# Optimization experiments

Hardware: AMD Instinct MI355X
Metric: run time of the kernel (lower is better)

The kernel has to match this reference:

```python
import jax, jax.numpy as jnp
import numpy as np

B, S, D, H, NK = 2, 512, 256, 8, 16
DK = D // H
NEG = -1e32


def _layer_norm(x, g, b, eps=1e-5):
    m = jnp.mean(x, axis=-1, keepdims=True)
    v = jnp.var(x, axis=-1, keepdims=True)
    return (x - m) / jnp.sqrt(v + eps) * g + b


def _attention(q, k, v, mask, gamma, maxout):
    # q,k,v: [b,h,s,dk]; mask: [1,1,s,s] bool; gamma: [h,1,1]
    d_k = q.shape[-1]
    scores = jnp.einsum('bhqd,bhkd->bhqk', q, k) / float(np.sqrt(d_k))
    s = scores.shape[-1]
    # gamma exp-decay branch (at=None in practice -> position_effect path)
    sm = jax.nn.softmax(jnp.where(mask, scores, NEG), axis=-1)
    distcum = jnp.cumsum(sm, axis=-1)
    disttotal = jnp.sum(sm, axis=-1, keepdims=True)
    idx = jnp.arange(s, dtype=scores.dtype)
    pos = jnp.abs(idx[None, :] - idx[:, None])[None, None]  # |x1 - x2|
    dist = jax.lax.stop_gradient(
        jnp.sqrt(jnp.clip((disttotal - distcum) * pos, 0.0, None)))
    g = -jnp.abs(gamma)[None]  # [1,h,1,1]
    total_effect = jnp.clip(jnp.exp(dist * g), 1e-5, 1e5)
    scores = scores * total_effect
    scores = jax.nn.softmax(jnp.where(mask, scores, NEG), axis=-1)
    scores = jnp.where(mask, scores, 0.0)
    if maxout:
        scale = jnp.minimum(1.0 / jnp.max(scores, axis=-1, keepdims=True), 5.0)
        scores = scores * scale
    out = jnp.einsum('bhqk,bhkd->bhqd', scores, v)
    return out, scores


def _mha(qx, kx, vx, mask, Wq, bq, Wk, bk, Wv, bv, Wo, bo, gammas, maxout):
    b, s, d = qx.shape
    def proj(x, W, bb):
        return (x @ W.T + bb).reshape(b, s, H, DK).transpose(0, 2, 1, 3)
    q = proj(qx, Wq, bq)
    k = proj(kx, Wk, bk)
    v = proj(vx, Wv, bv)
    out, scores = _attention(q, k, v, mask, gammas, maxout)
    concat = out.transpose(0, 2, 1, 3).reshape(b, s, d)
    return concat @ Wo.T + bo, scores


def _layer(qx, kx, vx, mask, Wq, bq, Wk, bk, Wv, bv, Wo, bo, gammas, ln_g, ln_b, maxout):
    out, scores = _mha(qx, kx, vx, mask, Wq, bq, Wk, bk, Wv, bv, Wo, bo, gammas, maxout)
    return _layer_norm(qx + out, ln_g, ln_b), scores  # dropout=identity in eval


def setup_inputs() -> dict:
    key = jax.random.key(0)
    ks = iter(jax.random.split(key, 40))
    def W(shp, sc=0.05):
        return jax.random.normal(next(ks), shp, jnp.float32) * sc
    return dict(
        q_emb=jax.random.normal(next(ks), (B, S, D), jnp.float32),
        s_emb=jax.random.normal(next(ks), (B, S, D), jnp.float32),
        s_emb_extr=jax.random.normal(next(ks), (B, S, D), jnp.float32),
        lens=jax.random.randint(next(ks), (B,), 1, S),
        at=jax.random.randint(next(ks), (B, S), 0, 300),
        Wq1=W((D, D)), bq1=jnp.zeros((D,)), Wv1=W((D, D)), bv1=jnp.zeros((D,)),
        Wo1=W((D, D)), bo1=jnp.zeros((D,)), gam1=W((H, 1, 1), 0.3),
        ln1_g=jnp.ones((D,)), ln1_b=jnp.zeros((D,)),
        Wq4=W((D, D)), bq4=jnp.zeros((D,)), Wk4=W((D, D)), bk4=jnp.zeros((D,)),
        Wv4=W((D, D)), bv4=jnp.zeros((D,)),
        Wo4=W((D, D)), bo4=jnp.zeros((D,)), gam4=W((H, 1, 1), 0.3),
        ln4_g=jnp.ones((D,)), ln4_b=jnp.zeros((D,)),
        know_params=jax.random.uniform(next(ks), (NK, D), jnp.float32, -1.0, 1.0),
    )


def reference(q_emb, s_emb, s_emb_extr, lens, at,
              Wq1, bq1, Wv1, bv1, Wo1, bo1, gam1, ln1_g, ln1_b,
              Wq4, bq4, Wk4, bk4, Wv4, bv4, Wo4, bo4, gam4, ln4_g, ln4_b,
              know_params):
    bs, s, d = q_emb.shape
    tri = jnp.tril(jnp.ones((s, s), bool), 0)[None, None]       # peek_cur=True
    tri_strict = jnp.tril(jnp.ones((s, s), bool), -1)[None, None]  # peek_cur=False
    # block1: kq_same -> k_linear is q_linear; maxout=False
    p, q_scores = _layer(q_emb, q_emb, s_emb, tri,
                         Wq1, bq1, Wq1, bq1, Wv1, bv1, Wo1, bo1, gam1,
                         ln1_g, ln1_b, maxout=False)
    # expand knowledge queries: [bs*NK, s, d]
    query = jnp.broadcast_to(know_params[None, :, None, :], (bs, NK, s, d)).reshape(bs * NK, s, d)
    hq = jnp.broadcast_to(q_emb[:, None], (bs, NK, s, d)).reshape(bs * NK, s, d)
    pe = jnp.broadcast_to(p[:, None], (bs, NK, s, d)).reshape(bs * NK, s, d)
    # block4: kq_same=False; maxout=True
    z, k_scores = _layer(query, hq, pe, tri_strict,
                         Wq4, bq4, Wk4, bk4, Wv4, bv4, Wo4, bo4, gam4,
                         ln4_g, ln4_b, maxout=True)
    z = z.reshape(bs, NK, s, d).transpose(0, 2, 1, 3).reshape(bs, s, NK * d)
    k_scores = k_scores.reshape(bs, NK, H, s, s).transpose(0, 2, 3, 1, 4)
    return z, q_scores, k_scores
```

## Files before the change

### kernel.cpp

```cpp
#include <hip/hip_runtime.h>


namespace {
constexpr int kB = 2, kS = 512, kD = 256, kH = 8, kDK = 32, kNK = 16;
constexpr float kScale = 0.17677669529663687f;
constexpr int kPS = 520;
constexpr int kSL = 528;
}

typedef unsigned short u16;
typedef u16 u16x4 __attribute__((ext_vector_type(4)));
typedef u16 u16x8 __attribute__((ext_vector_type(8)));
typedef short s16x8 __attribute__((ext_vector_type(8)));
typedef float f32x4 __attribute__((ext_vector_type(4)));

__device__ __forceinline__ float bf2f(u16 u) { return __uint_as_float(((unsigned)u) << 16); }
__device__ __forceinline__ u16 f2bf(float f) {
    unsigned u = __float_as_uint(f);
    return (u16)((u + 0x7fffu + ((u >> 16) & 1u)) >> 16);
}

__device__ __forceinline__ float wave_max64(float v) {
#pragma unroll
    for (int off = 32; off; off >>= 1) v = fmaxf(v, __shfl_xor(v, off));
    return v;
}
__device__ __forceinline__ float wave_sum64(float v) {
#pragma unroll
    for (int off = 32; off; off >>= 1) v += __shfl_xor(v, off);
    return v;
}

__global__ __launch_bounds__(256) void wt_kernel(const float* __restrict__ W0,
                                                 const float* __restrict__ W1,
                                                 const float* __restrict__ W2,
                                                 const float* __restrict__ W3,
                                                 const float* __restrict__ W4,
                                                 const float* __restrict__ W5,
                                                 const float* __restrict__ W6,
                                                 float* __restrict__ WT) {
    __shared__ float tile[32][33];
    const float* srcs[7] = {W0, W1, W2, W3, W4, W5, W6};
    const float* W = srcs[blockIdx.y];
    float* T = WT + (size_t)blockIdx.y * kD * kD;
    const int tx = blockIdx.x & 7, ty = blockIdx.x >> 3;
    const int t = threadIdx.x;
    {
        const int cl = t >> 3, kl = (t & 7) * 4;
        f32x4 v = *(const f32x4*)(W + (size_t)(ty * 32 + cl) * kD + tx * 32 + kl);
        tile[cl][kl] = v[0]; tile[cl][kl + 1] = v[1];
        tile[cl][kl + 2] = v[2]; tile[cl][kl + 3] = v[3];
    }
    __syncthreads();
    {
        const int kl = t >> 3, cl = (t & 7) * 4;
        f32x4 o = {tile[cl][kl], tile[cl + 1][kl], tile[cl + 2][kl], tile[cl + 3][kl]};
        *(f32x4*)(T + (size_t)(tx * 32 + kl) * kD + ty * 32 + cl) = o;
    }
}

__global__ __launch_bounds__(256) void gemm256_b4(const float* __restrict__ q_emb,
                                                  const float* __restrict__ s_emb,
                                                  const float* __restrict__ know,
                                                  const float* __restrict__ WTq1,
                                                  const float* __restrict__ bq1,
                                                  const float* __restrict__ WTv1,
                                                  const float* __restrict__ bv1,
                                                  const float* __restrict__ WTk4,
                                                  const float* __restrict__ bk4,
                                                  const float* __restrict__ WTq4,
                                                  const float* __restrict__ bq4,
                                                  float* __restrict__ Q1,
                                                  u16* __restrict__ Vtg1,
                                                  float* __restrict__ K4,
                                                  float* __restrict__ Q4) {
    const int mode = blockIdx.y;
    if (mode == 3 && blockIdx.x >= 4) return;
    __shared__ float xs[4][kD];
    const float* X = (mode == 1) ? s_emb : (mode == 3) ? know : q_emb;
    const float* WT = (mode == 0) ? WTq1 : (mode == 1) ? WTv1 : (mode == 2) ? WTk4 : WTq4;
    const float* bias = (mode == 0) ? bq1 : (mode == 1) ? bv1 : (mode == 2) ? bk4 : bq4;
    const int t = threadIdx.x;
    const int r0 = blockIdx.x * 4;

    {
        const int idx = t * 4;
        const int r = idx >> 8, c = idx & 255;
        *(f32x4*)&xs[r][c] = *(const f32x4*)(X + (size_t)(r0 + r) * kD + c);
    }
    __syncthreads();

    const int wv = t >> 6;
    const int c4 = (t & 63) * 4;
    float acc[4];
    {
        f32x4 bv = *(const f32x4*)(bias + c4);
#pragma unroll
        for (int j = 0; j < 4; ++j) acc[j] = bv[j];
    }
    for (int k0 = 0; k0 < kD; k0 += 4) {
        f32x4 w0 = *(const f32x4*)(WT + (size_t)(k0 + 0) * kD + c4);
        f32x4 w1 = *(const f32x4*)(WT + (size_t)(k0 + 1) * kD + c4);
        f32x4 w2 = *(const f32x4*)(WT + (size_t)(k0 + 2) * kD + c4);
        f32x4 w3 = *(const f32x4*)(WT + (size_t)(k0 + 3) * kD + c4);
        f32x4 xv = *(const f32x4*)&xs[wv][k0];
#pragma unroll
        for (int cc = 0; cc < 4; ++cc) {
            acc[cc] = fmaf(xv[0], w0[cc], acc[cc]);
            acc[cc] = fmaf(xv[1], w1[cc], acc[cc]);
            acc[cc] = fmaf(xv[2], w2[cc], acc[cc]);
            acc[cc] = fmaf(xv[3], w3[cc], acc[cc]);
        }
    }
    const int row = r0 + wv;
    if (mode == 3) {
        *(f32x4*)(Q4 + (size_t)row * kD + c4) = *(f32x4*)acc;
    } else if (mode == 1) {
        const int b = row >> 9, s = row & (kS - 1);
        const int h = c4 >> 5, dk = c4 & 31;
        u16* base = Vtg1 + (((size_t)(b * kH + h) * kDK + dk) * kS + s);
#pragma unroll
        for (int j = 0; j < 4; ++j) base[(size_t)j * kS] = f2bf(acc[j]);
    } else {
        float* Y = (mode == 0) ? Q1 : K4;
        const int h = c4 >> 5, dk = c4 & 31;
        *(f32x4*)(Y + (((size_t)(row >> 9) * kH + h) * kS + (row & (kS - 1))) * kDK + dk) =
            *(f32x4*)acc;
    }
}

__global__ __launch_bounds__(256) void epi1v4_kernel(const float* __restrict__ A1,
                                                     const float* __restrict__ qe,
                                                     const float* __restrict__ WTo1,
                                                     const float* __restrict__ bo1,
                                                     const float* __restrict__ lng,
                                                     const float* __restrict__ lnb,
                                                     const float* __restrict__ WTv4,
                                                     const float* __restrict__ bv4,
                                                     u16* __restrict__ Vtg) {
    __shared__ float xs[4][kD];
    __shared__ float ps[4][kD];
    const int t = threadIdx.x;
    const int r0 = blockIdx.x * 4;

    {
        const int chunk = t >> 3;
        const int r = chunk >> 3, h = chunk & 7;
        const int row = r0 + r;
        const float* src = A1 + (((size_t)(row >> 9) * kH + h) * kS + (row & (kS - 1))) * kDK + (t & 7) * 4;
        *(f32x4*)&xs[r][h * kDK + (t & 7) * 4] = *(const f32x4*)src;
    }
    __syncthreads();

    const int wv = t >> 6;
    const int c4 = (t & 63) * 4;
    const int row = r0 + wv;

    {
        float acc[4];
        f32x4 bv = *(const f32x4*)(bo1 + c4);
#pragma unroll
        for (int j = 0; j < 4; ++j) acc[j] = bv[j];
        for (int k0 = 0; k0 < kD; k0 += 4) {
            f32x4 w0 = *(const f32x4*)(WTo1 + (size_t)(k0 + 0) * kD + c4);
            f32x4 w1 = *(const f32x4*)(WTo1 + (size_t)(k0 + 1) * kD + c4);
            f32x4 w2 = *(const f32x4*)(WTo1 + (size_t)(k0 + 2) * kD + c4);
            f32x4 w3 = *(const f32x4*)(WTo1 + (size_t)(k0 + 3) * kD + c4);
            f32x4 xv = *(const f32x4*)&xs[wv][k0];
#pragma unroll
            for (int cc = 0; cc < 4; ++cc) {
                acc[cc] = fmaf(xv[0], w0[cc], acc[cc]);
                acc[cc] = fmaf(xv[1], w1[cc], acc[cc]);
                acc[cc] = fmaf(xv[2], w2[cc], acc[cc]);
                acc[cc] = fmaf(xv[3], w3[cc], acc[cc]);
            }
        }
        f32x4 e = *(const f32x4*)(qe + (size_t)row * kD + c4);
        f32x4 x;
#pragma unroll
        for (int j = 0; j < 4; ++j) x[j] = acc[j] + e[j];
        float s1 = x[0] + x[1] + x[2] + x[3];
        float s2 = x[0] * x[0] + x[1] * x[1] + x[2] * x[2] + x[3] * x[3];
#pragma unroll
        for (int off = 32; off; off >>= 1) {
            s1 += __shfl_xor(s1, off);
            s2 += __shfl_xor(s2, off);
        }
        const float mean = s1 * (1.f / kD);
        const float var = s2 * (1.f / kD) - mean * mean;
        const float rstd = rsqrtf(var + 1e-5f);
        f32x4 g = *(const f32x4*)(lng + c4);
        f32x4 bb = *(const f32x4*)(lnb + c4);
#pragma unroll
        for (int j = 0; j < 4; ++j) ps[wv][c4 + j] = (x[j] - mean) * rstd * g[j] + bb[j];
    }
    __syncthreads();

    {
        float acc[4];
        f32x4 bv = *(const f32x4*)(bv4 + c4);
#pragma unroll
        for (int j = 0; j < 4; ++j) acc[j] = bv[j];
        for (int k0 = 0; k0 < kD; k0 += 4) {
            f32x4 w0 = *(const f32x4*)(WTv4 + (size_t)(k0 + 0) * kD + c4);
            f32x4 w1 = *(const f32x4*)(WTv4 + (size_t)(k0 + 1) * kD + c4);
            f32x4 w2 = *(const f32x4*)(WTv4 + (size_t)(k0 + 2) * kD + c4);
            f32x4 w3 = *(const f32x4*)(WTv4 + (size_t)(k0 + 3) * kD + c4);
            f32x4 xv = *(const f32x4*)&ps[wv][k0];
#pragma unroll
            for (int cc = 0; cc < 4; ++cc) {
                acc[cc] = fmaf(xv[0], w0[cc], acc[cc]);
                acc[cc] = fmaf(xv[1], w1[cc], acc[cc]);
                acc[cc] = fmaf(xv[2], w2[cc], acc[cc]);
                acc[cc] = fmaf(xv[3], w3[cc], acc[cc]);
            }
        }
        const int b = row >> 9, s = row & (kS - 1);
        const int h = c4 >> 5, dk = c4 & 31;
        u16* base = Vtg + (((size_t)(b * kH + h) * kDK + dk) * kS + s);
#pragma unroll
        for (int j = 0; j < 4; ++j) base[(size_t)j * kS] = f2bf(acc[j]);
    }
}

template <int RPW, int MODE>
__global__ __launch_bounds__(256) void gemm256(const float* __restrict__ X,
                                               const float* __restrict__ WT,
                                               const float* __restrict__ bias,
                                               const float* __restrict__ extra,
                                               const float* __restrict__ lng,
                                               const float* __restrict__ lnb,
                                               float* __restrict__ Y) {
    constexpr int TM = RPW * 4;
    __shared__ float xs[TM][kD];
    const int t = threadIdx.x;
    const int r0 = blockIdx.x * TM;

    if (MODE == 0) {
#pragma unroll
        for (int it = 0; it < RPW; ++it) {
            const int idx = it * 1024 + t * 4;
            const int r = idx >> 8, c = idx & 255;
            *(f32x4*)&xs[r][c] = *(const f32x4*)(X + (size_t)(r0 + r) * kD + c);
        }
    } else {
#pragma unroll
        for (int it = 0; it < RPW; ++it) {
            const int chunk = it * 32 + (t >> 3);
            const int r = chunk >> 3, h = chunk & 7;
            const int row = r0 + r;
            const float* src = X + (((size_t)(row >> 9) * kH + h) * kS + (row & (kS - 1))) * kDK + (t & 7) * 4;
            *(f32x4*)&xs[r][h * kDK + (t & 7) * 4] = *(const f32x4*)src;
        }
    }
    __syncthreads();

    const int wv = t >> 6;
    const int c4 = (t & 63) * 4;
    float acc[RPW][4];
    {
        f32x4 bv = *(const f32x4*)(bias + c4);
#pragma unroll
        for (int r = 0; r < RPW; ++r)
#pragma unroll
            for (int j = 0; j < 4; ++j) acc[r][j] = bv[j];
    }
    for (int k0 = 0; k0 < kD; k0 += 4) {
        f32x4 w0 = *(const f32x4*)(WT + (size_t)(k0 + 0) * kD + c4);
        f32x4 w1 = *(const f32x4*)(WT + (size_t)(k0 + 1) * kD + c4);
        f32x4 w2 = *(const f32x4*)(WT + (size_t)(k0 + 2) * kD + c4);
        f32x4 w3 = *(const f32x4*)(WT + (size_t)(k0 + 3) * kD + c4);
#pragma unroll
        for (int r = 0; r < RPW; ++r) {
            f32x4 xv = *(const f32x4*)&xs[wv * RPW + r][k0];
#pragma unroll
            for (int cc = 0; cc < 4; ++cc) {
                acc[r][cc] = fmaf(xv[0], w0[cc], acc[r][cc]);
                acc[r][cc] = fmaf(xv[1], w1[cc], acc[r][cc]);
                acc[r][cc] = fmaf(xv[2], w2[cc], acc[r][cc]);
                acc[r][cc] = fmaf(xv[3], w3[cc], acc[r][cc]);
            }
        }
    }

#pragma unroll
    for (int r = 0; r < RPW; ++r) {
        const int row = r0 + wv * RPW + r;
        if (MODE == 0) {
            const int h = c4 >> 5, dk = c4 & 31;
            *(f32x4*)(Y + (((size_t)(row >> 9) * kH + h) * kS + (row & (kS - 1))) * kDK + dk) =
                *(f32x4*)acc[r];
        } else {
            f32x4 x;
            if (MODE == 1) {
                f32x4 e = *(const f32x4*)(extra + (size_t)row * kD + c4);
#pragma unroll
                for (int j = 0; j < 4; ++j) x[j] = acc[r][j] + e[j];
            } else {
                const int nk = (row >> 9) & (kNK - 1);
                f32x4 e = *(const f32x4*)(extra + (size_t)nk * kD + c4);
#pragma unroll
                for (int j = 0; j < 4; ++j) x[j] = acc[r][j] + e[j];
            }
            float s1 = x[0] + x[1] + x[2] + x[3];
            float s2 = x[0] * x[0] + x[1] * x[1] + x[2] * x[2] + x[3] * x[3];
#pragma unroll
            for (int off = 32; off; off >>= 1) {
                s1 += __shfl_xor(s1, off);
                s2 += __shfl_xor(s2, off);
            }
            const float mean = s1 * (1.f / kD);
            const float var = s2 * (1.f / kD) - mean * mean;
            const float rstd = rsqrtf(var + 1e-5f);
            f32x4 g = *(const f32x4*)(lng + c4);
            f32x4 bb = *(const f32x4*)(lnb + c4);
            f32x4 y;
#pragma unroll
            for (int j = 0; j < 4; ++j) y[j] = (x[j] - mean) * rstd * g[j] + bb[j];
            if (MODE == 1) {
                *(f32x4*)(Y + (size_t)row * kD + c4) = y;
            } else {
                const int bnk = row >> 9, s = row & (kS - 1);
                const int nk = bnk & (kNK - 1), b = bnk >> 4;
                *(f32x4*)(Y + (((size_t)(b * kS + s) * kNK + nk) * kD) + c4) = y;
            }
        }
    }
}

__global__ __launch_bounds__(256) void attn1_prep_kernel(const float* __restrict__ Q1,
                                                         const u16* __restrict__ Vtg1,
                                                         const float* __restrict__ gam,
                                                         const float* __restrict__ Q4,
                                                         const float* __restrict__ K4,
                                                         float* __restrict__ rawP,
                                                         float* __restrict__ CpreP,
                                                         float* __restrict__ q_scores,
                                                         float* __restrict__ A1) {
    extern __shared__ char smem[];
    const int bx = blockIdx.x;
    const int tid = threadIdx.x;
    const int lane = tid & 63;
    const int w = tid >> 6;

    if (bx >= kB * kH * (kS / 16)) {
        const int panel = (bx - kB * kH * (kS / 16)) * 4 + w;
        const int h = panel & (kH - 1);
        const int bnk = panel >> 3;
        const int nk = bnk & (kNK - 1);
        const int b = bnk >> 4;
        const float* Kp = K4 + (size_t)(b * kH + h) * kS * kDK;
        float qv[kDK];
        const float* Qr = Q4 + (size_t)nk * kD + h * kDK;
#pragma unroll
        for (int d = 0; d < kDK; ++d) qv[d] = Qr[d];

        const int k0 = lane * 8;
        float raw[8];
        float m = -3e38f;
#pragma unroll
        for (int j = 0; j < 8; ++j) {
            const float* kr = Kp + (size_t)(k0 + j) * kDK;
            float s = 0.f;
#pragma unroll
            for (int d4 = 0; d4 < 8; ++d4) {
                f32x4 kv = *(const f32x4*)(kr + d4 * 4);
                s = fmaf(qv[d4 * 4 + 0], kv[0], s);
                s = fmaf(qv[d4 * 4 + 1], kv[1], s);
                s = fmaf(qv[d4 * 4 + 2], kv[2], s);
                s = fmaf(qv[d4 * 4 + 3], kv[3], s);
            }
            raw[j] = s * kScale;
            m = fmaxf(m, raw[j]);
        }
        m = wave_max64(m);
        float E[8];
        float s = 0.f;
#pragma unroll
        for (int j = 0; j < 8; ++j) { E[j] = __expf(raw[j] - m); s += E[j]; }
        float inc = s;
#pragma unroll
        for (int off = 1; off < 64; off <<= 1) {
            float t2 = __shfl_up(inc, off);
            if (lane >= off) inc += t2;
        }
        float run = inc - s;
        float cp[8];
#pragma unroll
        for (int j = 0; j < 8; ++j) { run += E[j]; cp[j] = run; }

        float* rrow = rawP + (size_t)panel * kS + k0;
        float* crow = CpreP + (size_t)panel * kS + k0;
        *(f32x4*)(rrow) = *(f32x4*)(raw);
        *(f32x4*)(rrow + 4) = *(f32x4*)(raw + 4);
        *(f32x4*)(crow) = *(f32x4*)(cp);
        *(f32x4*)(crow + 4) = *(f32x4*)(cp + 4);
        return;
    }

    float* Sl = (float*)smem;
    u16* Pl = (u16*)smem;

    const int bh = bx >> 5;
    const int q0 = (bx & 31) * 16;
    const int h = bh & (kH - 1);
    const float* Kb = Q1 + (size_t)bh * kS * kDK;

    {
        const int qrow = q0 + (lane & 15);
        const int dof = (lane >> 4) * 8;
        f32x4 qa = *(const f32x4*)(Kb + (size_t)qrow * kDK + dof);
        f32x4 qb = *(const f32x4*)(Kb + (size_t)qrow * kDK + dof + 4);
        s16x8 aq_h, aq_l;
#pragma unroll
        for (int j = 0; j < 4; ++j) {
            float f = qa[j];
            u16 hi = f2bf(f);
            aq_h[j] = (short)hi;
            aq_l[j] = (short)f2bf(f - bf2f(hi));
            f = qb[j];
            hi = f2bf(f);
            aq_h[4 + j] = (short)hi;
            aq_l[4 + j] = (short)f2bf(f - bf2f(hi));
        }
        for (int kt = w * 8; kt < w * 8 + 8; ++kt) {
            const int krow = kt * 16 + (lane & 15);
            f32x4 ka = *(const f32x4*)(Kb + (size_t)krow * kDK + dof);
            f32x4 kb2 = *(const f32x4*)(Kb + (size_t)krow * kDK + dof + 4);
            s16x8 bk_h, bk_l;
#pragma unroll
            for (int j = 0; j < 4; ++j) {
                float f = ka[j];
                u16 hi = f2bf(f);
                bk_h[j] = (short)hi;
                bk_l[j] = (short)f2bf(f - bf2f(hi));
                f = kb2[j];
                hi = f2bf(f);
                bk_h[4 + j] = (short)hi;
                bk_l[4 + j] = (short)f2bf(f - bf2f(hi));
            }
            f32x4 acc = {0.f, 0.f, 0.f, 0.f};
            acc = __builtin_amdgcn_mfma_f32_16x16x32_bf16(aq_h, bk_h, acc, 0, 0, 0);
            acc = __builtin_amdgcn_mfma_f32_16x16x32_bf16(aq_l, bk_h, acc, 0, 0, 0);
            acc = __builtin_amdgcn_mfma_f32_16x16x32_bf16(aq_h, bk_l, acc, 0, 0, 0);
            const int colk = kt * 16 + (lane & 15);
            const int seg = colk >> 5, ii = colk & 31;
#pragma unroll
            for (int j = 0; j < 4; ++j) {
                const int row = (lane >> 4) * 4 + j;
                Sl[row * kSL + seg * 33 + ii] = acc[j] * kScale;
            }
        }
    }
    __syncthreads();

    const float gh = -fabsf(gam[h]);
    const int r = tid >> 4, seg16 = tid & 15;
    const int q = q0 + r, L = q + 1, ks = seg16 * 32;
    float sv[32];
    {
        const float* srow = Sl + r * kSL + seg16 * 33;
#pragma unroll
        for (int i = 0; i < 32; ++i) sv[i] = srow[i];
    }
    __syncthreads();
    {
        const int nv = min(max(L - ks, 0), 32);
        float m = -3e38f;
#pragma unroll
        for (int i = 0; i < 32; ++i)
            if (i < nv) m = fmaxf(m, sv[i]);
#pragma unroll
        for (int off = 1; off < 16; off <<= 1) m = fmaxf(m, __shfl_xor(m, off));
        float segsum = 0.f;
#pragma unroll
        for (int i = 0; i < 32; ++i)
            if (i < nv) segsum += __expf(sv[i] - m);
        float tot = segsum;
#pragma unroll
        for (int off = 1; off < 16; off <<= 1) tot += __shfl_xor(tot, off);
        float inc = segsum;
#pragma unroll
        for (int off = 1; off < 16; off <<= 1) {
            const float tmp = __shfl_up(inc, off);
            if ((tid & 15) >= off) inc += tmp;
        }
        float run = inc - segsum;
        const float inv_tot = 1.f / tot;
        float m2 = -3e38f;
#pragma unroll
        for (int i = 0; i < 32; ++i) {
            if (i < nv) {
                const float E = __expf(sv[i] - m);
                run += E;
                const float rem = 1.f - run * inv_tot;
                const float pos = (float)(q - (ks + i));
                const float val = fmaxf(rem * pos, 0.f);
                const float te = fmaxf(__expf(gh * sqrtf(val)), 1e-5f);
                const float s2 = sv[i] * te;
                sv[i] = s2;
                m2 = fmaxf(m2, s2);
            }
        }
#pragma unroll
        for (int off = 1; off < 16; off <<= 1) m2 = fmaxf(m2, __shfl_xor(m2, off));
        float sum2 = 0.f;
#pragma unroll
        for (int i = 0; i < 32; ++i) {
            const float p = (i < nv) ? __expf(sv[i] - m2) : 0.f;
            sv[i] = p;
            sum2 += p;
        }
#pragma unroll
        for (int off = 1; off < 16; off <<= 1) sum2 += __shfl_xor(sum2, off);
        const float inv2 = 1.f / sum2;
        float* qrow = q_scores + ((size_t)bh * kS + q) * kS + ks;
        u16* prow = Pl + r * kPS + ks;
#pragma unroll
        for (int i = 0; i < 32; i += 4) {
            f32x4 o;
            u16x4 pb;
#pragma unroll
            for (int j = 0; j < 4; ++j) {
                const float p = sv[i + j] * inv2;
                o[j] = p;
                pb[j] = f2bf(p);
            }
            *(f32x4*)(qrow + i) = o;
            *(u16x4*)(prow + i) = pb;
        }
    }
    __syncthreads();

    if (w < 2) {
        const int dt = w;
        const u16* Arow = Pl + (size_t)(lane & 15) * kPS + (lane >> 4) * 8;
        const u16* Brow = Vtg1 + ((size_t)bh * kDK + dt * 16 + (lane & 15)) * kS + (lane >> 4) * 8;
        f32x4 acc = {0.f, 0.f, 0.f, 0.f};
#pragma unroll
        for (int kc = 0; kc < kS; kc += 32) {
            s16x8 a = *(const s16x8*)(Arow + kc);
            s16x8 b = *(const s16x8*)(Brow + kc);
            acc = __builtin_amdgcn_mfma_f32_16x16x32_bf16(a, b, acc, 0, 0, 0);
        }
        const int d = dt * 16 + (lane & 15);
#pragma unroll
        for (int j = 0; j < 4; ++j) {
            const int row = (lane >> 4) * 4 + j;
            A1[((size_t)bh * kS + (q0 + row)) * kDK + d] = acc[j];
        }
    }
}

__global__ __launch_bounds__(256) void attn4_main(const float* __restrict__ rawP,
                                                  const float* __restrict__ CpreP,
                                                  const u16* __restrict__ Vtg,
                                                  const float* __restrict__ gam,
                                                  float* __restrict__ k_scores,
                                                  float* __restrict__ A4) {
    extern __shared__ char smem[];
    u16* Pl = (u16*)smem;
    float* raws_l = (float*)(smem + 32 * kPS * 2);
    float* cps_l = raws_l + kS;

    const int panel = blockIdx.x;
    const int q0 = blockIdx.y * 32;
    const int h = panel & (kH - 1);
    const int bnk = panel >> 3;
    const int nk = bnk & (kNK - 1);
    const int b = bnk >> 4;
    const int tid = threadIdx.x;
    const int lane = tid & 63;
    const int w = tid >> 6;

    for (int i = tid; i < kS; i += 256) {
        raws_l[i] = rawP[(size_t)panel * kS + i];
        cps_l[i] = CpreP[(size_t)panel * kS + i];
    }
    __syncthreads();

    const float gh = -fabsf(gam[h]);
    const int rbase = w * 8;
    const int k0 = lane * 8;
    float rw[8], cp[8];
    *(f32x4*)(rw) = *(const f32x4*)(raws_l + k0);
    *(f32x4*)(rw + 4) = *(const f32x4*)(raws_l + k0 + 4);
    *(f32x4*)(cp) = *(const f32x4*)(cps_l + k0);
    *(f32x4*)(cp + 4) = *(const f32x4*)(cps_l + k0 + 4);

    for (int r = 0; r < 8; ++r) {
        const int row = rbase + r;
        const int Lr = q0 + row;
        float* krow = k_scores + ((size_t)((b * kH + h) * kS + Lr) * kNK + nk) * kS;
        u16* prow = Pl + (size_t)row * kPS + k0;
        if (Lr == 0) {
            f32x4 z = {0.f, 0.f, 0.f, 0.f};
            *(f32x4*)(krow + k0) = z;
            *(f32x4*)(krow + k0 + 4) = z;
            u16x8 zb = {0, 0, 0, 0, 0, 0, 0, 0};
            *(u16x8*)(prow) = zb;
            continue;
        }
        const float invCL = 1.f / cps_l[Lr - 1];
        const float fL = (float)(Lr - k0);
        float s2v[8];
        float mloc = -3e38f;
#pragma unroll
        for (int j = 0; j < 8; ++j) {
            const float rem = 1.f - cp[j] * invCL;
            const float val = fmaxf(rem * (fL - (float)j), 0.f);
            const float te = fmaxf(__expf(gh * sqrtf(val)), 1e-5f);
            const float s2 = rw[j] * te;
            s2v[j] = s2;
            if (k0 + j < Lr) mloc = fmaxf(mloc, s2);
        }
        const float m2 = wave_max64(mloc);
        float p[8];
        float psum = 0.f;
#pragma unroll
        for (int j = 0; j < 8; ++j) {
            p[j] = (k0 + j < Lr) ? __expf(s2v[j] - m2) : 0.f;
            psum += p[j];
        }
        const float sum2 = wave_sum64(psum);
        const float scl = fminf(sum2, 5.f) / sum2;
        u16x8 pb;
#pragma unroll
        for (int j = 0; j < 8; ++j) {
            p[j] *= scl;
            pb[j] = f2bf(p[j]);
        }
        *(f32x4*)(krow + k0) = *(f32x4*)(p);
        *(f32x4*)(krow + k0 + 4) = *(f32x4*)(p + 4);
        *(u16x8*)(prow) = pb;
    }
    __syncthreads();

    const int rowblk = (w & 1) * 16;
    const int dblk = (w >> 1) * 16;
    const u16* Arow = Pl + (size_t)(rowblk + (lane & 15)) * kPS + (lane >> 4) * 8;
    const u16* Brow = Vtg + ((size_t)(b * kH + h) * kDK + dblk + (lane & 15)) * kS + (lane >> 4) * 8;
    f32x4 acc = {0.f, 0.f, 0.f, 0.f};
#pragma unroll
    for (int kc = 0; kc < kS; kc += 32) {
        s16x8 a = *(const s16x8*)(Arow + kc);
        s16x8 bfr = *(const s16x8*)(Brow + kc);
        acc = __builtin_amdgcn_mfma_f32_16x16x32_bf16(a, bfr, acc, 0, 0, 0);
    }
    const int d = dblk + (lane & 15);
#pragma unroll
    for (int j = 0; j < 4; ++j) {
        const int row = rowblk + (lane >> 4) * 4 + j;
        A4[((size_t)panel * kS + (q0 + row)) * kDK + d] = acc[j];
    }
}

extern "C" void kernel_launch(void* const* d_in, const int* in_sizes, int n_in,
                              void* d_out, int out_size, void* d_ws, size_t ws_size,
                              hipStream_t stream) {
    (void)in_sizes; (void)n_in; (void)out_size; (void)ws_size;

    const float* q_emb = (const float*)d_in[0];
    const float* s_emb = (const float*)d_in[1];
    const float* Wq1 = (const float*)d_in[5];  const float* bq1 = (const float*)d_in[6];
    const float* Wv1 = (const float*)d_in[7];  const float* bv1 = (const float*)d_in[8];
    const float* Wo1 = (const float*)d_in[9];  const float* bo1 = (const float*)d_in[10];
    const float* gam1 = (const float*)d_in[11];
    const float* ln1g = (const float*)d_in[12]; const float* ln1b = (const float*)d_in[13];
    const float* Wq4 = (const float*)d_in[14]; const float* bq4 = (const float*)d_in[15];
    const float* Wk4 = (const float*)d_in[16]; const float* bk4 = (const float*)d_in[17];
    const float* Wv4 = (const float*)d_in[18]; const float* bv4 = (const float*)d_in[19];
    const float* Wo4 = (const float*)d_in[20]; const float* bo4 = (const float*)d_in[21];
    const float* gam4 = (const float*)d_in[22];
    const float* ln4g = (const float*)d_in[23]; const float* ln4b = (const float*)d_in[24];
    const float* know = (const float*)d_in[25];

    float* ws = (float*)d_ws;
    const size_t NBHSD = (size_t)kB * kH * kS * kDK;
    float* Q1 = ws;
    float* RAW = Q1 + NBHSD;
    float* A1 = RAW + NBHSD;
    float* K4 = A1 + NBHSD;
    float* Q4 = K4 + NBHSD;
    float* A4 = Q4 + (size_t)kNK * kD;
    float* WT = A4 + (size_t)kB * kNK * kH * kS * kDK;
    u16* Vtg = (u16*)(WT + 7 * (size_t)kD * kD);
    u16* Vtg1 = Vtg + (size_t)kB * kH * kDK * kS;

    float* rawP = RAW;
    float* CpreP = RAW + (size_t)kB * kNK * kH * kS;

    float* WTq1 = WT + 0 * (size_t)kD * kD;
    float* WTv1 = WT + 1 * (size_t)kD * kD;
    float* WTo1 = WT + 2 * (size_t)kD * kD;
    float* WTk4 = WT + 3 * (size_t)kD * kD;
    float* WTv4 = WT + 4 * (size_t)kD * kD;
    float* WTo4 = WT + 5 * (size_t)kD * kD;
    float* WTq4 = WT + 6 * (size_t)kD * kD;

    float* zout = (float*)d_out;
    float* q_scores = zout + (size_t)kB * kS * kNK * kD;
    float* k_scores = q_scores + (size_t)kB * kH * kS * kS;

    {
        dim3 g(64, 7);
        wt_kernel<<<g, 256, 0, stream>>>(Wq1, Wv1, Wo1, Wk4, Wv4, Wo4, Wq4, WT);
    }
    {
        dim3 g(kB * kS / 4, 4);
        gemm256_b4<<<g, 256, 0, stream>>>(q_emb, s_emb, know,
                                          WTq1, bq1, WTv1, bv1, WTk4, bk4, WTq4, bq4,
                                          Q1, Vtg1, K4, Q4);
    }
    {
        const int nb1 = kB * kH * (kS / 16);
        const int nbp = kB * kNK * kH / 4;
        const int lds1 = 16 * kSL * 4;
        attn1_prep_kernel<<<nb1 + nbp, 256, lds1, stream>>>(Q1, Vtg1, gam1, Q4, K4,
                                                            rawP, CpreP, q_scores, A1);
    }
    epi1v4_kernel<<<kB * kS / 4, 256, 0, stream>>>(A1, q_emb, WTo1, bo1, ln1g, ln1b,
                                                   WTv4, bv4, Vtg);
    {
        dim3 g5(kB * kNK * kH, kS / 32);
        const int lds_bytes = 32 * kPS * 2 + 2 * kS * 4;
        attn4_main<<<g5, 256, lds_bytes, stream>>>(rawP, CpreP, Vtg, gam4, k_scores, A4);
    }
    gemm256<4, 2><<<kB * kNK * kS / 16, 256, 0, stream>>>(A4, WTo4, bo4, know, ln4g, ln4b, zout);
}
```

Before: 215.7 us.

## Retile projection GEMMs so each wave covers 64 columns across multiple rows

The fp32 projection GEMMs (gemm b4, epi1v4, epi4) now map each wave to a 64-column slice and each lane to four columns across several rows, instead of one wave per row spanning all 256 columns. Each weight row load is therefore reused across four rows per lane, and gemmb4 grows from 4 to 16 rows per block. This cuts global weight traffic per output. The layer-norm row reduction now needs a cross-wave LDS reduction with an extra barrier, and gemmb4 launches fewer blocks.

```diff
diff --git a/kernel.cpp b/kernel.cpp
--- a/kernel.cpp
+++ b/kernel.cpp
@@ -59,73 +59,76 @@
     }
 }
 
-__global__ __launch_bounds__(256) void gemm256_b4(const float* __restrict__ q_emb,
-                                                  const float* __restrict__ s_emb,
-                                                  const float* __restrict__ know,
-                                                  const float* __restrict__ WTq1,
-                                                  const float* __restrict__ bq1,
-                                                  const float* __restrict__ WTv1,
-                                                  const float* __restrict__ bv1,
-                                                  const float* __restrict__ WTk4,
-                                                  const float* __restrict__ bk4,
-                                                  const float* __restrict__ WTq4,
-                                                  const float* __restrict__ bq4,
-                                                  float* __restrict__ Q1,
-                                                  u16* __restrict__ Vtg1,
-                                                  float* __restrict__ K4,
-                                                  float* __restrict__ Q4) {
+__global__ __launch_bounds__(256) void gemmb4(const float* __restrict__ q_emb,
+                                              const float* __restrict__ s_emb,
+                                              const float* __restrict__ know,
+                                              const float* __restrict__ WTq1,
+                                              const float* __restrict__ bq1,
+                                              const float* __restrict__ WTv1,
+                                              const float* __restrict__ bv1,
+                                              const float* __restrict__ WTk4,
+                                              const float* __restrict__ bk4,
+                                              const float* __restrict__ WTq4,
+                                              const float* __restrict__ bq4,
+                                              float* __restrict__ Q1,
+                                              u16* __restrict__ Vtg1,
+                                              float* __restrict__ K4,
+                                              float* __restrict__ Q4) {
     const int mode = blockIdx.y;
-    if (mode == 3 && blockIdx.x >= 4) return;
-    __shared__ float xs[4][kD];
+    if (mode == 3 && blockIdx.x >= 1) return;
+    __shared__ float xs[16][kD];
     const float* X = (mode == 1) ? s_emb : (mode == 3) ? know : q_emb;
     const float* WT = (mode == 0) ? WTq1 : (mode == 1) ? WTv1 : (mode == 2) ? WTk4 : WTq4;
     const float* bias = (mode == 0) ? bq1 : (mode == 1) ? bv1 : (mode == 2) ? bk4 : bq4;
     const int t = threadIdx.x;
-    const int r0 = blockIdx.x * 4;
-
-    {
-        const int idx = t * 4;
+    const int r0 = blockIdx.x * 16;
+
+#pragma unroll
+    for (int it = 0; it < 4; ++it) {
+        const int idx = it * 1024 + t * 4;
         const int r = idx >> 8, c = idx & 255;
         *(f32x4*)&xs[r][c] = *(const f32x4*)(X + (size_t)(r0 + r) * kD + c);
     }
     __syncthreads();
 
-    const int wv = t >> 6;
-    const int c4 = (t & 63) * 4;
-    float acc[4];
+    const int w = t >> 6, l = t & 63;
+    const int rb = (l >> 4) * 4;
+    const int c4 = w * 64 + (l & 15) * 4;
+    f32x4 acc[4];
     {
         f32x4 bv = *(const f32x4*)(bias + c4);
 #pragma unroll
-        for (int j = 0; j < 4; ++j) acc[j] = bv[j];
+        for (int rr = 0; rr < 4; ++rr) acc[rr] = bv;
     }
     for (int k0 = 0; k0 < kD; k0 += 4) {
         f32x4 w0 = *(const f32x4*)(WT + (size_t)(k0 + 0) * kD + c4);
         f32x4 w1 = *(const f32x4*)(WT + (size_t)(k0 + 1) * kD + c4);
         f32x4 w2 = *(const f32x4*)(WT + (size_t)(k0 + 2) * kD + c4);
         f32x4 w3 = *(const f32x4*)(WT + (size_t)(k0 + 3) * kD + c4);
-        f32x4 xv = *(const f32x4*)&xs[wv][k0];
-#pragma unroll
-        for (int cc = 0; cc < 4; ++cc) {
-            acc[cc] = fmaf(xv[0], w0[cc], acc[cc]);
-            acc[cc] = fmaf(xv[1], w1[cc], acc[cc]);
-            acc[cc] = fmaf(xv[2], w2[cc], acc[cc]);
-            acc[cc] = fmaf(xv[3], w3[cc], acc[cc]);
-        }
-    }
-    const int row = r0 + wv;
-    if (mode == 3) {
-        *(f32x4*)(Q4 + (size_t)row * kD + c4) = *(f32x4*)acc;
-    } else if (mode == 1) {
-        const int b = row >> 9, s = row & (kS - 1);
-        const int h = c4 >> 5, dk = c4 & 31;
-        u16* base = Vtg1 + (((size_t)(b * kH + h) * kDK + dk) * kS + s);
-#pragma unroll
-        for (int j = 0; j < 4; ++j) base[(size_t)j * kS] = f2bf(acc[j]);
-    } else {
-        float* Y = (mode == 0) ? Q1 : K4;
-        const int h = c4 >> 5, dk = c4 & 31;
-        *(f32x4*)(Y + (((size_t)(row >> 9) * kH + h) * kS + (row & (kS - 1))) * kDK + dk) =
-            *(f32x4*)acc;
+#pragma unroll
+        for (int rr = 0; rr < 4; ++rr) {
+            f32x4 xv = *(const f32x4*)&xs[rb + rr][k0];
+            acc[rr] += xv[0] * w0 + xv[1] * w1 + xv[2] * w2 + xv[3] * w3;
+        }
+    }
+
+#pragma unroll
+    for (int rr = 0; rr < 4; ++rr) {
+        const int row = r0 + rb + rr;
+        if (mode == 3) {
+            *(f32x4*)(Q4 + (size_t)row * kD + c4) = acc[rr];
+        } else if (mode == 1) {
+            const int b = row >> 9, s = row & (kS - 1);
+            const int h = c4 >> 5, dk = c4 & 31;
+            u16* base = Vtg1 + (((size_t)(b * kH + h) * kDK + dk) * kS + s);
+#pragma unroll
+            for (int j = 0; j < 4; ++j) base[(size_t)j * kS] = f2bf(acc[rr][j]);
+        } else {
+            float* Y = (mode == 0) ? Q1 : K4;
+            const int h = c4 >> 5, dk = c4 & 31;
+            *(f32x4*)(Y + (((size_t)(row >> 9) * kH + h) * kS + (row & (kS - 1))) * kDK + dk) =
+                acc[rr];
+        }
     }
 }
 
@@ -140,6 +143,7 @@
                                                      u16* __restrict__ Vtg) {
     __shared__ float xs[4][kD];
     __shared__ float ps[4][kD];
+    __shared__ float red[4][4][2];
     const int t = threadIdx.x;
     const int r0 = blockIdx.x * 4;
 
@@ -152,70 +156,55 @@
     }
     __syncthreads();
 
-    const int wv = t >> 6;
-    const int c4 = (t & 63) * 4;
-    const int row = r0 + wv;
-
-    {
-        float acc[4];
-        f32x4 bv = *(const f32x4*)(bo1 + c4);
-#pragma unroll
-        for (int j = 0; j < 4; ++j) acc[j] = bv[j];
+    const int w = t >> 6, l = t & 63;
+    const int row = l >> 4;
+    const int c4 = w * 64 + (l & 15) * 4;
+    const int grow = r0 + row;
+
+    {
+        f32x4 acc = *(const f32x4*)(bo1 + c4);
         for (int k0 = 0; k0 < kD; k0 += 4) {
             f32x4 w0 = *(const f32x4*)(WTo1 + (size_t)(k0 + 0) * kD + c4);
             f32x4 w1 = *(const f32x4*)(WTo1 + (size_t)(k0 + 1) * kD + c4);
             f32x4 w2 = *(const f32x4*)(WTo1 + (size_t)(k0 + 2) * kD + c4);
             f32x4 w3 = *(const f32x4*)(WTo1 + (size_t)(k0 + 3) * kD + c4);
-            f32x4 xv = *(const f32x4*)&xs[wv][k0];
-#pragma unroll
-            for (int cc = 0; cc < 4; ++cc) {
-                acc[cc] = fmaf(xv[0], w0[cc], acc[cc]);
-                acc[cc] = fmaf(xv[1], w1[cc], acc[cc]);
-                acc[cc] = fmaf(xv[2], w2[cc], acc[cc]);
-                acc[cc] = fmaf(xv[3], w3[cc], acc[cc]);
-            }
-        }
-        f32x4 e = *(const f32x4*)(qe + (size_t)row * kD + c4);
-        f32x4 x;
-#pragma unroll
-        for (int j = 0; j < 4; ++j) x[j] = acc[j] + e[j];
+            f32x4 xv = *(const f32x4*)&xs[row][k0];
+            acc += xv[0] * w0 + xv[1] * w1 + xv[2] * w2 + xv[3] * w3;
+        }
+        f32x4 e = *(const f32x4*)(qe + (size_t)grow * kD + c4);
+        f32x4 x = acc + e;
         float s1 = x[0] + x[1] + x[2] + x[3];
         float s2 = x[0] * x[0] + x[1] * x[1] + x[2] * x[2] + x[3] * x[3];
 #pragma unroll
-        for (int off = 32; off; off >>= 1) {
+        for (int off = 1; off < 16; off <<= 1) {
             s1 += __shfl_xor(s1, off);
             s2 += __shfl_xor(s2, off);
         }
-        const float mean = s1 * (1.f / kD);
-        const float var = s2 * (1.f / kD) - mean * mean;
+        if ((l & 15) == 0) { red[w][row][0] = s1; red[w][row][1] = s2; }
+        __syncthreads();
+        const float sum = red[0][row][0] + red[1][row][0] + red[2][row][0] + red[3][row][0];
+        const float sq = red[0][row][1] + red[1][row][1] + red[2][row][1] + red[3][row][1];
+        const float mean = sum * (1.f / kD);
+        const float var = sq * (1.f / kD) - mean * mean;
         const float rstd = rsqrtf(var + 1e-5f);
         f32x4 g = *(const f32x4*)(lng + c4);
         f32x4 bb = *(const f32x4*)(lnb + c4);
 #pragma unroll
-        for (int j = 0; j < 4; ++j) ps[wv][c4 + j] = (x[j] - mean) * rstd * g[j] + bb[j];
-    }
-    __syncthreads();
-
-    {
-        float acc[4];
-        f32x4 bv = *(const f32x4*)(bv4 + c4);
-#pragma unroll
-        for (int j = 0; j < 4; ++j) acc[j] = bv[j];
+        for (int j = 0; j < 4; ++j) ps[row][c4 + j] = (x[j] - mean) * rstd * g[j] + bb[j];
+    }
+    __syncthreads();
+
+    {
+        f32x4 acc = *(const f32x4*)(bv4 + c4);
         for (int k0 = 0; k0 < kD; k0 += 4) {
             f32x4 w0 = *(const f32x4*)(WTv4 + (size_t)(k0 + 0) * kD + c4);
             f32x4 w1 = *(const f32x4*)(WTv4 + (size_t)(k0 + 1) * kD + c4);
             f32x4 w2 = *(const f32x4*)(WTv4 + (size_t)(k0 + 2) * kD + c4);
             f32x4 w3 = *(const f32x4*)(WTv4 + (size_t)(k0 + 3) * kD + c4);
-            f32x4 xv = *(const f32x4*)&ps[wv][k0];
-#pragma unroll
-            for (int cc = 0; cc < 4; ++cc) {
-                acc[cc] = fmaf(xv[0], w0[cc], acc[cc]);
-                acc[cc] = fmaf(xv[1], w1[cc], acc[cc]);
-                acc[cc] = fmaf(xv[2], w2[cc], acc[cc]);
-                acc[cc] = fmaf(xv[3], w3[cc], acc[cc]);
-            }
-        }
-        const int b = row >> 9, s = row & (kS - 1);
+            f32x4 xv = *(const f32x4*)&ps[row][k0];
+            acc += xv[0] * w0 + xv[1] * w1 + xv[2] * w2 + xv[3] * w3;
+        }
+        const int b = grow >> 9, s = grow & (kS - 1);
         const int h = c4 >> 5, dk = c4 & 31;
         u16* base = Vtg + (((size_t)(b * kH + h) * kDK + dk) * kS + s);
 #pragma unroll
@@ -223,108 +212,82 @@
     }
 }
 
-template <int RPW, int MODE>
-__global__ __launch_bounds__(256) void gemm256(const float* __restrict__ X,
-                                               const float* __restrict__ WT,
-                                               const float* __restrict__ bias,
-                                               const float* __restrict__ extra,
-                                               const float* __restrict__ lng,
-                                               const float* __restrict__ lnb,
-                                               float* __restrict__ Y) {
-    constexpr int TM = RPW * 4;
-    __shared__ float xs[TM][kD];
+__global__ __launch_bounds__(256) void epi4_kernel(const float* __restrict__ A4,
+                                                   const float* __restrict__ WTo4,
+                                                   const float* __restrict__ bo4,
+                                                   const float* __restrict__ know,
+                                                   const float* __restrict__ lng,
+                                                   const float* __restrict__ lnb,
+                                                   float* __restrict__ zout) {
+    __shared__ float xs[16][kD];
+    __shared__ float red[4][16][2];
     const int t = threadIdx.x;
-    const int r0 = blockIdx.x * TM;
-
-    if (MODE == 0) {
-#pragma unroll
-        for (int it = 0; it < RPW; ++it) {
-            const int idx = it * 1024 + t * 4;
-            const int r = idx >> 8, c = idx & 255;
-            *(f32x4*)&xs[r][c] = *(const f32x4*)(X + (size_t)(r0 + r) * kD + c);
-        }
-    } else {
-#pragma unroll
-        for (int it = 0; it < RPW; ++it) {
-            const int chunk = it * 32 + (t >> 3);
-            const int r = chunk >> 3, h = chunk & 7;
-            const int row = r0 + r;
-            const float* src = X + (((size_t)(row >> 9) * kH + h) * kS + (row & (kS - 1))) * kDK + (t & 7) * 4;
-            *(f32x4*)&xs[r][h * kDK + (t & 7) * 4] = *(const f32x4*)src;
-        }
-    }
-    __syncthreads();
-
-    const int wv = t >> 6;
-    const int c4 = (t & 63) * 4;
-    float acc[RPW][4];
-    {
-        f32x4 bv = *(const f32x4*)(bias + c4);
-#pragma unroll
-        for (int r = 0; r < RPW; ++r)
-#pragma unroll
-            for (int j = 0; j < 4; ++j) acc[r][j] = bv[j];
+    const int r0 = blockIdx.x * 16;
+
+#pragma unroll
+    for (int it = 0; it < 4; ++it) {
+        const int chunk = it * 32 + (t >> 3);
+        const int r = chunk >> 3, h = chunk & 7;
+        const int row = r0 + r;
+        const float* src = A4 + (((size_t)(row >> 9) * kH + h) * kS + (row & (kS - 1))) * kDK + (t & 7) * 4;
+        *(f32x4*)&xs[r][h * kDK + (t & 7) * 4] = *(const f32x4*)src;
+    }
+    __syncthreads();
+
+    const int w = t >> 6, l = t & 63;
+    const int rb = (l >> 4) * 4;
+    const int c4 = w * 64 + (l & 15) * 4;
+    f32x4 acc[4];
+    {
+        f32x4 bv = *(const f32x4*)(bo4 + c4);
+#pragma unroll
+        for (int rr = 0; rr < 4; ++rr) acc[rr] = bv;
     }
     for (int k0 = 0; k0 < kD; k0 += 4) {
-        f32x4 w0 = *(const f32x4*)(WT + (size_t)(k0 + 0) * kD + c4);
-        f32x4 w1 = *(const f32x4*)(WT + (size_t)(k0 + 1) * kD + c4);
-        f32x4 w2 = *(const f32x4*)(WT + (size_t)(k0 + 2) * kD + c4);
-        f32x4 w3 = *(const f32x4*)(WT + (size_t)(k0 + 3) * kD + c4);
-#pragma unroll
-        for (int r = 0; r < RPW; ++r) {
-            f32x4 xv = *(const f32x4*)&xs[wv * RPW + r][k0];
-#pragma unroll
-            for (int cc = 0; cc < 4; ++cc) {
-                acc[r][cc] = fmaf(xv[0], w0[cc], acc[r][cc]);
-                acc[r][cc] = fmaf(xv[1], w1[cc], acc[r][cc]);
-                acc[r][cc] = fmaf(xv[2], w2[cc], acc[r][cc]);
-                acc[r][cc] = fmaf(xv[3], w3[cc], acc[r][cc]);
-            }
-        }
-    }
-
-#pragma unroll
-    for (int r = 0; r < RPW; ++r) {
-        const int row = r0 + wv * RPW + r;
-        if (MODE == 0) {
-            const int h = c4 >> 5, dk = c4 & 31;
-            *(f32x4*)(Y + (((size_t)(row >> 9) * kH + h) * kS + (row & (kS - 1))) * kDK + dk) =
-                *(f32x4*)acc[r];
-        } else {
-            f32x4 x;
-            if (MODE == 1) {
-                f32x4 e = *(const f32x4*)(extra + (size_t)row * kD + c4);
-#pragma unroll
-                for (int j = 0; j < 4; ++j) x[j] = acc[r][j] + e[j];
-            } else {
-                const int nk = (row >> 9) & (kNK - 1);
-                f32x4 e = *(const f32x4*)(extra + (size_t)nk * kD + c4);
-#pragma unroll
-                for (int j = 0; j < 4; ++j) x[j] = acc[r][j] + e[j];
-            }
-            float s1 = x[0] + x[1] + x[2] + x[3];
-            float s2 = x[0] * x[0] + x[1] * x[1] + x[2] * x[2] + x[3] * x[3];
-#pragma unroll
-            for (int off = 32; off; off >>= 1) {
-                s1 += __shfl_xor(s1, off);
-                s2 += __shfl_xor(s2, off);
-            }
-            const float mean = s1 * (1.f / kD);
-            const float var = s2 * (1.f / kD) - mean * mean;
-            const float rstd = rsqrtf(var + 1e-5f);
-            f32x4 g = *(const f32x4*)(lng + c4);
-            f32x4 bb = *(const f32x4*)(lnb + c4);
-            f32x4 y;
-#pragma unroll
-            for (int j = 0; j < 4; ++j) y[j] = (x[j] - mean) * rstd * g[j] + bb[j];
-            if (MODE == 1) {
-                *(f32x4*)(Y + (size_t)row * kD + c4) = y;
-            } else {
-                const int bnk = row >> 9, s = row & (kS - 1);
-                const int nk = bnk & (kNK - 1), b = bnk >> 4;
-                *(f32x4*)(Y + (((size_t)(b * kS + s) * kNK + nk) * kD) + c4) = y;
-            }
-        }
+        f32x4 w0 = *(const f32x4*)(WTo4 + (size_t)(k0 + 0) * kD + c4);
+        f32x4 w1 = *(const f32x4*)(WTo4 + (size_t)(k0 + 1) * kD + c4);
+        f32x4 w2 = *(const f32x4*)(WTo4 + (size_t)(k0 + 2) * kD + c4);
+        f32x4 w3 = *(const f32x4*)(WTo4 + (size_t)(k0 + 3) * kD + c4);
+#pragma unroll
+        for (int rr = 0; rr < 4; ++rr) {
+            f32x4 xv = *(const f32x4*)&xs[rb + rr][k0];
+            acc[rr] += xv[0] * w0 + xv[1] * w1 + xv[2] * w2 + xv[3] * w3;
+        }
+    }
+
+    f32x4 x[4];
+#pragma unroll
+    for (int rr = 0; rr < 4; ++rr) {
+        const int row = r0 + rb + rr;
+        const int nk = (row >> 9) & (kNK - 1);
+        f32x4 e = *(const f32x4*)(know + (size_t)nk * kD + c4);
+        x[rr] = acc[rr] + e;
+        float s1 = x[rr][0] + x[rr][1] + x[rr][2] + x[rr][3];
+        float s2 = x[rr][0] * x[rr][0] + x[rr][1] * x[rr][1] + x[rr][2] * x[rr][2] + x[rr][3] * x[rr][3];
+#pragma unroll
+        for (int off = 1; off < 16; off <<= 1) {
+            s1 += __shfl_xor(s1, off);
+            s2 += __shfl_xor(s2, off);
+        }
+        if ((l & 15) == 0) { red[w][rb + rr][0] = s1; red[w][rb + rr][1] = s2; }
+    }
+    __syncthreads();
+    f32x4 g = *(const f32x4*)(lng + c4);
+    f32x4 bb = *(const f32x4*)(lnb + c4);
+#pragma unroll
+    for (int rr = 0; rr < 4; ++rr) {
+        const int row = r0 + rb + rr;
+        const float sum = red[0][rb + rr][0] + red[1][rb + rr][0] + red[2][rb + rr][0] + red[3][rb + rr][0];
+        const float sq = red[0][rb + rr][1] + red[1][rb + rr][1] + red[2][rb + rr][1] + red[3][rb + rr][1];
+        const float mean = sum * (1.f / kD);
+        const float var = sq * (1.f / kD) - mean * mean;
+        const float rstd = rsqrtf(var + 1e-5f);
+        f32x4 y;
+#pragma unroll
+        for (int j = 0; j < 4; ++j) y[j] = (x[rr][j] - mean) * rstd * g[j] + bb[j];
+        const int bnk = row >> 9, s = row & (kS - 1);
+        const int nk = bnk & (kNK - 1), b = bnk >> 4;
+        *(f32x4*)(zout + (((size_t)(b * kS + s) * kNK + nk) * kD) + c4) = y;
     }
 }
 
@@ -707,10 +670,10 @@
         wt_kernel<<<g, 256, 0, stream>>>(Wq1, Wv1, Wo1, Wk4, Wv4, Wo4, Wq4, WT);
     }
     {
-        dim3 g(kB * kS / 4, 4);
-        gemm256_b4<<<g, 256, 0, stream>>>(q_emb, s_emb, know,
-                                          WTq1, bq1, WTv1, bv1, WTk4, bk4, WTq4, bq4,
-                                          Q1, Vtg1, K4, Q4);
+        dim3 g(kB * kS / 16, 4);
+        gemmb4<<<g, 256, 0, stream>>>(q_emb, s_emb, know,
+                                      WTq1, bq1, WTv1, bv1, WTk4, bk4, WTq4, bq4,
+                                      Q1, Vtg1, K4, Q4);
     }
     {
         const int nb1 = kB * kH * (kS / 16);
@@ -726,5 +689,5 @@
         const int lds_bytes = 32 * kPS * 2 + 2 * kS * 4;
         attn4_main<<<g5, 256, lds_bytes, stream>>>(rawP, CpreP, Vtg, gam4, k_scores, A4);
     }
-    gemm256<4, 2><<<kB * kNK * kS / 16, 256, 0, stream>>>(A4, WTo4, bo4, know, ln4g, ln4b, zout);
-}
+    epi4_kernel<<<kB * kNK * kS / 16, 256, 0, stream>>>(A4, WTo4, bo4, know, ln4g, ln4b, zout);
+}
```

After: 229.9 us. 6.6% more time.
